# Performance work log

Hardware: AMD Instinct MI355X
Metric: run time of the kernel (lower is better)

## Reference

```python
import jax, jax.numpy as jnp
import numpy as np
import math

N = 8192
DIM = 256

def setup_inputs() -> dict:
    key = jax.random.key(0)
    k1, k2, k3 = jax.random.split(key, 3)
    h = jax.random.normal(k1, (N, DIM), dtype=jnp.float32)
    # xavier_uniform with gain=1.414 for square [dim, dim] matrices
    gain = 1.414
    bound = gain * math.sqrt(6.0 / (DIM + DIM))
    Wq = jax.random.uniform(k2, (DIM, DIM), dtype=jnp.float32, minval=-bound, maxval=bound)
    Wk = jax.random.uniform(k3, (DIM, DIM), dtype=jnp.float32, minval=-bound, maxval=bound)
    return {"h": h, "Wq": Wq, "Wk": Wk}

def reference(h, Wq, Wk):
    dim = h.shape[1]
    q = h @ Wq                                   # [N, dim]
    k = h @ Wk                                   # [N, dim]
    e = (q @ k.T) / jnp.sqrt(jnp.asarray(dim, h.dtype))  # [N, N]
    attention = jax.nn.softmax(e, axis=1)        # row-wise softmax
    attention = attention.mean(axis=0)           # [N], column-mean over rows
    x = attention @ h                            # [dim]
    return x
```

## Files before the change

### kernel.cpp

```cpp
#include <hip/hip_runtime.h>
#include <cstdint>
#include <cstddef>


#define N_ROWS 8192
#define DIM    256

typedef __bf16 bf16x8 __attribute__((ext_vector_type(8)));
typedef unsigned short u16x8 __attribute__((ext_vector_type(8)));
typedef float f32x16 __attribute__((ext_vector_type(16)));

__device__ __forceinline__ uint16_t f2bf(float f) {
    uint32_t u = __float_as_uint(f);
    uint32_t r = (u + 0x7fffu + ((u >> 16) & 1u)) >> 16;
    return (uint16_t)r;
}

__device__ __forceinline__ float fexp2(float x) {
#if __has_builtin(__builtin_amdgcn_exp2f)
    return __builtin_amdgcn_exp2f(x);
#else
    return __expf(x * 0.69314718056f);
#endif
}

__device__ __forceinline__ void gld16(const void* gsrc, void* ldst) {
    __builtin_amdgcn_global_load_lds(
        (const __attribute__((address_space(1))) unsigned int*)gsrc,
        (__attribute__((address_space(3))) unsigned int*)ldst, 16, 0, 0);
}

__global__ __launch_bounds__(256) void proj_kernel(
        const float* __restrict__ h, const float* __restrict__ Wq,
        const float* __restrict__ Wk, uint16_t* __restrict__ qf,
        uint16_t* __restrict__ kf, float* __restrict__ l_arr,
        float* __restrict__ c_arr, float* __restrict__ out) {
    __shared__ alignas(16) float hbf[32 * 260];
    __shared__ alignas(16) uint16_t rep[4][1024];
    const int tid = threadIdx.x, lane = tid & 63, wave = tid >> 6;
    const int bid = blockIdx.x;
    const int rt = bid >> 2, ph = bid & 3;
    const int which = ph >> 1, p = ph & 1;

    if (bid < 32)       l_arr[bid * 256 + tid] = 0.0f;
    else if (bid < 64)  c_arr[(bid - 32) * 256 + tid] = 0.0f;
    else if (bid == 64) out[tid] = 0.0f;

    const float* __restrict__ W = which ? Wk : Wq;
    uint16_t* __restrict__ dst = which ? kf : qf;
    const float scale = which ? 1.0f : (0.0625f * 1.44269504089f);

    for (int i = tid; i < 2048; i += 256) {
        int r = i >> 6, c = (i & 63) * 4;
        *(float4*)&hbf[r * 260 + c] = *(const float4*)&h[(size_t)(rt * 32 + r) * DIM + c];
    }
    __syncthreads();

    bf16x8 afrag[16];
    {
        const int r = lane & 31;
#pragma unroll
        for (int a0 = 0; a0 < 16; a0++) {
            const int c0 = a0 * 16 + (lane >> 5) * 8;
            float4 f0 = *(const float4*)&hbf[r * 260 + c0];
            float4 f1 = *(const float4*)&hbf[r * 260 + c0 + 4];
            u16x8 f;
            f[0] = f2bf(f0.x); f[1] = f2bf(f0.y); f[2] = f2bf(f0.z); f[3] = f2bf(f0.w);
            f[4] = f2bf(f1.x); f[5] = f2bf(f1.y); f[6] = f2bf(f1.z); f[7] = f2bf(f1.w);
            afrag[a0] = __builtin_bit_cast(bf16x8, f);
        }
    }

    const int ctl = wave;
    const int cl = ctl * 32 + (lane & 31);
    f32x16 acc;
#pragma unroll
    for (int i = 0; i < 16; i++) acc[i] = 0.0f;
#pragma unroll
    for (int a0 = 0; a0 < 16; a0++) {
        const int kb = a0 * 16 + (lane >> 5) * 8;
        u16x8 f;
#pragma unroll
        for (int j = 0; j < 8; j++)
            f[j] = f2bf(W[(size_t)(kb + j) * DIM + p * 128 + cl]);
        acc = __builtin_amdgcn_mfma_f32_32x32x16_bf16(
            afrag[a0], __builtin_bit_cast(bf16x8, f), acc, 0, 0, 0);
    }

    {
        const int dcl = lane & 31;
        const int a0o = dcl >> 4, hi = (dcl >> 3) & 1, jj = dcl & 7;
        const int ilb = 4 * (lane >> 5);
#pragma unroll
        for (int reg = 0; reg < 16; reg++) {
            int il = ilb + (reg & 3) + 8 * (reg >> 2);
            rep[wave][(size_t)((a0o * 64) + il + 32 * hi) * 8 + jj] =
                f2bf(acc[reg] * scale);
        }
        const uint4* rv = (const uint4*)&rep[wave][0];
        uint4* gp = (uint4*)(dst + (size_t)rt * 8192 +
                             (size_t)(p * 4 + ctl) * 1024);
        gp[lane * 2]     = rv[lane * 2];
        gp[lane * 2 + 1] = rv[lane * 2 + 1];
    }
}

template <int MODE>
__global__ __launch_bounds__(512, 2) void qk_pass(
        const uint16_t* __restrict__ qf, const uint16_t* __restrict__ kf,
        float* __restrict__ l_arr, float* __restrict__ c_arr) {
    __shared__ alignas(16) uint16_t ktile[2][16384];
    __shared__ float c_lds[512];
    const int tid = threadIdx.x, lane = tid & 63, wave = tid >> 6;
    const int bid = blockIdx.x;
    const int cc = bid & 15, rb = bid >> 4;
    const int t0 = rb * 16 + wave * 2;
    const int row0 = t0 * 32;

    const uint4* qp = (const uint4*)qf;
    bf16x8 q0[16], q1[16];
#pragma unroll
    for (int a0 = 0; a0 < 16; a0++) {
        q0[a0] = __builtin_bit_cast(bf16x8, qp[(size_t)t0 * 1024 + a0 * 64 + lane]);
        q1[a0] = __builtin_bit_cast(bf16x8, qp[(size_t)(t0 + 1) * 1024 + a0 * 64 + lane]);
    }

    float rs0[16], rs1[16];
    float rr0[16], rr1[16];
    if (MODE == 0) {
#pragma unroll
        for (int r = 0; r < 16; r++) { rs0[r] = 0.0f; rs1[r] = 0.0f; }
    } else {
#pragma unroll
        for (int r = 0; r < 16; r++) {
            int ro = (r & 3) + 8 * (r >> 2) + 4 * (lane >> 5);
            rr0[r] = 1.0f / (8192.0f * l_arr[row0 + ro]);
            rr1[r] = 1.0f / (8192.0f * l_arr[row0 + 32 + ro]);
        }
        if (tid < 512) c_lds[tid] = 0.0f;
    }

    const char* ksrc = (const char*)kf + (size_t)cc * 16 * 16384;

    {
        const char* s0 = ksrc + wave * 4096 + lane * 16;
        char* d0 = (char*)&ktile[0][0] + wave * 4096;
#pragma unroll
        for (int it = 0; it < 4; it++) gld16(s0 + it * 1024, d0 + it * 1024);
    }

    for (int g = 0; g < 8; g++) {
        __syncthreads();
        if (g < 7) {
            const char* sn = ksrc + (size_t)(2 * g + 2) * 16384 + wave * 4096 + lane * 16;
            char* dn = (char*)&ktile[(g + 1) & 1][0] + wave * 4096;
#pragma unroll
            for (int it = 0; it < 4; it++) gld16(sn + it * 1024, dn + it * 1024);
        }

#pragma unroll
        for (int sub = 0; sub < 2; sub++) {
            const int t = 2 * g + sub;
            const uint16_t* kt = &ktile[g & 1][sub * 8192];
            f32x16 acc0, acc1;
#pragma unroll
            for (int i = 0; i < 16; i++) { acc0[i] = 0.0f; acc1[i] = 0.0f; }
#pragma unroll
            for (int a0 = 0; a0 < 16; a0++) {
                bf16x8 b = __builtin_bit_cast(bf16x8,
                    *(const u16x8*)&kt[(size_t)(a0 * 64 + lane) * 8]);
                acc0 = __builtin_amdgcn_mfma_f32_32x32x16_bf16(q0[a0], b, acc0, 0, 0, 0);
                acc1 = __builtin_amdgcn_mfma_f32_32x32x16_bf16(q1[a0], b, acc1, 0, 0, 0);
            }

            if (MODE == 0) {
#pragma unroll
                for (int r = 0; r < 16; r++) {
                    rs0[r] += fexp2(acc0[r]);
                    rs1[r] += fexp2(acc1[r]);
                }
            } else {
                float sv = 0.0f;
#pragma unroll
                for (int r = 0; r < 16; r++) {
                    sv += fexp2(acc0[r]) * rr0[r];
                    sv += fexp2(acc1[r]) * rr1[r];
                }
                sv += __shfl_xor(sv, 32);
                if (lane < 32) atomicAdd(&c_lds[t * 32 + lane], sv);
            }
        }
    }

    if (MODE == 0) {
#pragma unroll
        for (int r = 0; r < 16; r++) {
            float v0 = rs0[r], v1 = rs1[r];
            v0 += __shfl_xor(v0, 1);  v0 += __shfl_xor(v0, 2);
            v0 += __shfl_xor(v0, 4);  v0 += __shfl_xor(v0, 8);
            v0 += __shfl_xor(v0, 16);
            v1 += __shfl_xor(v1, 1);  v1 += __shfl_xor(v1, 2);
            v1 += __shfl_xor(v1, 4);  v1 += __shfl_xor(v1, 8);
            v1 += __shfl_xor(v1, 16);
            if ((lane & 31) == 0) {
                int ro = (r & 3) + 8 * (r >> 2) + 4 * (lane >> 5);
                atomicAdd(&l_arr[row0 + ro], v0);
                atomicAdd(&l_arr[row0 + 32 + ro], v1);
            }
        }
    } else {
        __syncthreads();
        if (tid < 512) atomicAdd(&c_arr[cc * 512 + tid], c_lds[tid]);
    }
}

__global__ __launch_bounds__(256) void finish_kernel(
        const float* __restrict__ h, const float* __restrict__ c_arr,
        float* __restrict__ out) {
    const int d = threadIdx.x;
    const int j0 = blockIdx.x * 32;
    float acc = 0.0f;
#pragma unroll
    for (int jj = 0; jj < 32; jj++)
        acc += c_arr[j0 + jj] * h[(size_t)(j0 + jj) * DIM + d];
    atomicAdd(&out[d], acc);
}

extern "C" void kernel_launch(void* const* d_in, const int* in_sizes, int n_in,
                              void* d_out, int out_size, void* d_ws, size_t ws_size,
                              hipStream_t stream) {
    const float* h  = (const float*)d_in[0];
    const float* Wq = (const float*)d_in[1];
    const float* Wk = (const float*)d_in[2];

    uint16_t* qf = (uint16_t*)d_ws;
    uint16_t* kf = qf + (size_t)N_ROWS * DIM;
    float* l_arr = (float*)((char*)d_ws + (size_t)8 * 1024 * 1024);
    float* c_arr = l_arr + N_ROWS;
    float* out = (float*)d_out;

    proj_kernel<<<1024, 256, 0, stream>>>(h, Wq, Wk, qf, kf, l_arr, c_arr, out);
    qk_pass<0><<<256, 512, 0, stream>>>(qf, kf, l_arr, c_arr);
    qk_pass<1><<<256, 512, 0, stream>>>(qf, kf, l_arr, c_arr);
    finish_kernel<<<256, 256, 0, stream>>>(h, c_arr, out);
}
```

Measured before the change: 148.9 us.

## Store exp scores as fp16 matrix instead of recomputing QK^T in second pass

Replaces the two-pass scheme, which computed Q·K^T twice (once for row sums, once for the weighted column sums), with a single pass. That pass writes exp scores as an fp16 N×N matrix while it accumulates row sums. A new column-reduce kernel then reads the stored matrix, weights each entry by the inverse row sum, and accumulates column sums. This removes half of the MFMA work but adds a 128 MB write and read of the score matrix. The accumulators start at -9, a fixed exponent offset so values fit fp16, and values are clamped at 60000, which risks precision loss on large logits.

```diff
diff --git a/kernel.cpp b/kernel.cpp
--- a/kernel.cpp
+++ b/kernel.cpp
@@ -22,6 +22,13 @@
 #else
     return __expf(x * 0.69314718056f);
 #endif
+}
+
+__device__ __forceinline__ uint32_t pk_f16(float lo, float hi) {
+    union { _Float16 h[2]; uint32_t u; } v;
+    v.h[0] = (_Float16)lo;
+    v.h[1] = (_Float16)hi;
+    return v.u;
 }
 
 __device__ __forceinline__ void gld16(const void* gsrc, void* ldst) {
@@ -105,12 +112,10 @@
     }
 }
 
-template <int MODE>
-__global__ __launch_bounds__(512, 2) void qk_pass(
+__global__ __launch_bounds__(512, 2) void qk_store(
         const uint16_t* __restrict__ qf, const uint16_t* __restrict__ kf,
-        float* __restrict__ l_arr, float* __restrict__ c_arr) {
+        uint16_t* __restrict__ Pm, float* __restrict__ l_arr) {
     __shared__ alignas(16) uint16_t ktile[2][16384];
-    __shared__ float c_lds[512];
     const int tid = threadIdx.x, lane = tid & 63, wave = tid >> 6;
     const int bid = blockIdx.x;
     const int cc = bid & 15, rb = bid >> 4;
@@ -126,19 +131,11 @@
     }
 
     float rs0[16], rs1[16];
-    float rr0[16], rr1[16];
-    if (MODE == 0) {
-#pragma unroll
-        for (int r = 0; r < 16; r++) { rs0[r] = 0.0f; rs1[r] = 0.0f; }
-    } else {
-#pragma unroll
-        for (int r = 0; r < 16; r++) {
-            int ro = (r & 3) + 8 * (r >> 2) + 4 * (lane >> 5);
-            rr0[r] = 1.0f / (8192.0f * l_arr[row0 + ro]);
-            rr1[r] = 1.0f / (8192.0f * l_arr[row0 + 32 + ro]);
-        }
-        if (tid < 512) c_lds[tid] = 0.0f;
-    }
+#pragma unroll
+    for (int r = 0; r < 16; r++) { rs0[r] = 0.0f; rs1[r] = 0.0f; }
+
+    uint4* pst0 = (uint4*)(Pm + ((size_t)t0 * 256 + cc * 16) * 1024) + (size_t)lane * 2;
+    uint4* pst1 = pst0 + 256 * 128;
 
     const char* ksrc = (const char*)kf + (size_t)cc * 16 * 16384;
 
@@ -164,7 +161,7 @@
             const uint16_t* kt = &ktile[g & 1][sub * 8192];
             f32x16 acc0, acc1;
 #pragma unroll
-            for (int i = 0; i < 16; i++) { acc0[i] = 0.0f; acc1[i] = 0.0f; }
+            for (int i = 0; i < 16; i++) { acc0[i] = -9.0f; acc1[i] = -9.0f; }
 #pragma unroll
             for (int a0 = 0; a0 < 16; a0++) {
                 bf16x8 b = __builtin_bit_cast(bf16x8,
@@ -173,44 +170,96 @@
                 acc1 = __builtin_amdgcn_mfma_f32_32x32x16_bf16(q1[a0], b, acc1, 0, 0, 0);
             }
 
-            if (MODE == 0) {
-#pragma unroll
-                for (int r = 0; r < 16; r++) {
-                    rs0[r] += fexp2(acc0[r]);
-                    rs1[r] += fexp2(acc1[r]);
-                }
-            } else {
-                float sv = 0.0f;
-#pragma unroll
-                for (int r = 0; r < 16; r++) {
-                    sv += fexp2(acc0[r]) * rr0[r];
-                    sv += fexp2(acc1[r]) * rr1[r];
-                }
-                sv += __shfl_xor(sv, 32);
-                if (lane < 32) atomicAdd(&c_lds[t * 32 + lane], sv);
+            {
+                uint4 pw; float ea, eb;
+#define EPK(ACC, RS, J0, M)                                              \
+                ea = fminf(fexp2(ACC[J0]), 60000.0f);                    \
+                eb = fminf(fexp2(ACC[(J0) + 1]), 60000.0f);              \
+                RS[J0] += ea; RS[(J0) + 1] += eb;                        \
+                pw.M = pk_f16(ea, eb);
+                EPK(acc0, rs0, 0, x) EPK(acc0, rs0, 2, y)
+                EPK(acc0, rs0, 4, z) EPK(acc0, rs0, 6, w)
+                pst0[t * 128] = pw;
+                EPK(acc0, rs0, 8, x) EPK(acc0, rs0, 10, y)
+                EPK(acc0, rs0, 12, z) EPK(acc0, rs0, 14, w)
+                pst0[t * 128 + 1] = pw;
+                EPK(acc1, rs1, 0, x) EPK(acc1, rs1, 2, y)
+                EPK(acc1, rs1, 4, z) EPK(acc1, rs1, 6, w)
+                pst1[t * 128] = pw;
+                EPK(acc1, rs1, 8, x) EPK(acc1, rs1, 10, y)
+                EPK(acc1, rs1, 12, z) EPK(acc1, rs1, 14, w)
+                pst1[t * 128 + 1] = pw;
+#undef EPK
             }
         }
     }
 
-    if (MODE == 0) {
-#pragma unroll
-        for (int r = 0; r < 16; r++) {
-            float v0 = rs0[r], v1 = rs1[r];
-            v0 += __shfl_xor(v0, 1);  v0 += __shfl_xor(v0, 2);
-            v0 += __shfl_xor(v0, 4);  v0 += __shfl_xor(v0, 8);
-            v0 += __shfl_xor(v0, 16);
-            v1 += __shfl_xor(v1, 1);  v1 += __shfl_xor(v1, 2);
-            v1 += __shfl_xor(v1, 4);  v1 += __shfl_xor(v1, 8);
-            v1 += __shfl_xor(v1, 16);
-            if ((lane & 31) == 0) {
-                int ro = (r & 3) + 8 * (r >> 2) + 4 * (lane >> 5);
-                atomicAdd(&l_arr[row0 + ro], v0);
-                atomicAdd(&l_arr[row0 + 32 + ro], v1);
+#pragma unroll
+    for (int r = 0; r < 16; r++) {
+        float v0 = rs0[r], v1 = rs1[r];
+        v0 += __shfl_xor(v0, 1);  v0 += __shfl_xor(v0, 2);
+        v0 += __shfl_xor(v0, 4);  v0 += __shfl_xor(v0, 8);
+        v0 += __shfl_xor(v0, 16);
+        v1 += __shfl_xor(v1, 1);  v1 += __shfl_xor(v1, 2);
+        v1 += __shfl_xor(v1, 4);  v1 += __shfl_xor(v1, 8);
+        v1 += __shfl_xor(v1, 16);
+        if ((lane & 31) == 0) {
+            int ro = (r & 3) + 8 * (r >> 2) + 4 * (lane >> 5);
+            atomicAdd(&l_arr[row0 + ro], v0);
+            atomicAdd(&l_arr[row0 + 32 + ro], v1);
+        }
+    }
+}
+
+__global__ __launch_bounds__(512) void colreduce_kernel(
+        const uint16_t* __restrict__ Pm, const float* __restrict__ l_arr,
+        float* __restrict__ c_arr) {
+    __shared__ float wlds[128];
+    const int tid = threadIdx.x, lane = tid & 63, wave = tid >> 6;
+    const int bid = blockIdx.x;
+    const int cc = bid & 15, rg = bid >> 4;
+    if (tid < 128) wlds[tid] = 1.0f / (8192.0f * l_arr[rg * 128 + tid]);
+    __syncthreads();
+
+    const int rbase = 16 * (lane & 1);
+    float acc0 = 0.0f, acc1 = 0.0f;
+#pragma unroll
+    for (int t = 0; t < 4; t++) {
+        float wA[8], wB[8];
+#pragma unroll
+        for (int j = 0; j < 8; j++) {
+            const int r = (j & 3) + 8 * (j >> 2) + rbase;
+            wA[j] = wlds[t * 32 + r];
+            wB[j] = wlds[t * 32 + r + 4];
+        }
+        const size_t trow = (size_t)(rg * 4 + t) * 256;
+#pragma unroll
+        for (int c = 0; c < 2; c++) {
+            const uint4* up = (const uint4*)(Pm + (trow + cc * 16 + wave * 2 + c) * 1024);
+            uint4 v0 = up[lane];
+            uint4 v1 = up[lane + 64];
+            uint32_t a[4] = {v0.x, v0.y, v0.z, v0.w};
+            uint32_t b[4] = {v1.x, v1.y, v1.z, v1.w};
+            float s = 0.0f;
+#pragma unroll
+            for (int j = 0; j < 4; j++) {
+                union { uint32_t u; _Float16 h[2]; } ta, tb;
+                ta.u = a[j]; tb.u = b[j];
+                s += (float)ta.h[0] * wA[2 * j]
+                   + (float)ta.h[1] * wA[2 * j + 1]
+                   + (float)tb.h[0] * wB[2 * j]
+                   + (float)tb.h[1] * wB[2 * j + 1];
             }
-        }
-    } else {
-        __syncthreads();
-        if (tid < 512) atomicAdd(&c_arr[cc * 512 + tid], c_lds[tid]);
+            if (c == 0) acc0 += s; else acc1 += s;
+        }
+    }
+
+    acc0 += __shfl_xor(acc0, 1);
+    acc1 += __shfl_xor(acc1, 1);
+    if ((lane & 1) == 0) {
+        const int col = lane >> 1;
+        atomicAdd(&c_arr[cc * 512 + (wave * 2 + 0) * 32 + col], acc0);
+        atomicAdd(&c_arr[cc * 512 + (wave * 2 + 1) * 32 + col], acc1);
     }
 }
 
@@ -237,10 +286,11 @@
     uint16_t* kf = qf + (size_t)N_ROWS * DIM;
     float* l_arr = (float*)((char*)d_ws + (size_t)8 * 1024 * 1024);
     float* c_arr = l_arr + N_ROWS;
+    uint16_t* Pm = (uint16_t*)((char*)d_ws + (size_t)16 * 1024 * 1024);
     float* out = (float*)d_out;
 
     proj_kernel<<<1024, 256, 0, stream>>>(h, Wq, Wk, qf, kf, l_arr, c_arr, out);
-    qk_pass<0><<<256, 512, 0, stream>>>(qf, kf, l_arr, c_arr);
-    qk_pass<1><<<256, 512, 0, stream>>>(qf, kf, l_arr, c_arr);
+    qk_store<<<256, 512, 0, stream>>>(qf, kf, Pm, l_arr);
+    colreduce_kernel<<<1024, 512, 0, stream>>>(Pm, l_arr, c_arr);
     finish_kernel<<<256, 256, 0, stream>>>(h, c_arr, out);
 }
```

Result: slower. 185.3 us (+24.4%).

## Fuse two QK passes into one cooperative kernel with grid sync

Applied to the files above, without the earlier changes.

Merges the row-sum pass and the column-accumulation pass into a single cooperative kernel separated by a grid-wide barrier. Q fragments stay in registers across both phases, and the first K tile for the second pass is prefetched before the barrier. This removes one kernel launch and the reload of Q. In exchange it adds a grid sync and requires all 256 blocks to be co-resident.

```diff
diff --git a/kernel.cpp b/kernel.cpp
--- a/kernel.cpp
+++ b/kernel.cpp
@@ -1,6 +1,9 @@
 #include <hip/hip_runtime.h>
+#include <hip/hip_cooperative_groups.h>
 #include <cstdint>
 #include <cstddef>
+
+namespace cg = cooperative_groups;
 
 
 #define N_ROWS 8192
@@ -105,8 +108,7 @@
     }
 }
 
-template <int MODE>
-__global__ __launch_bounds__(512, 2) void qk_pass(
+__global__ __launch_bounds__(512, 2) void qk_fused(
         const uint16_t* __restrict__ qf, const uint16_t* __restrict__ kf,
         float* __restrict__ l_arr, float* __restrict__ c_arr) {
     __shared__ alignas(16) uint16_t ktile[2][16384];
@@ -125,42 +127,30 @@
         q1[a0] = __builtin_bit_cast(bf16x8, qp[(size_t)(t0 + 1) * 1024 + a0 * 64 + lane]);
     }
 
+    const char* ksrc = (const char*)kf + (size_t)cc * 16 * 16384;
+    const char* kwsrc = ksrc + wave * 4096 + lane * 16;
+    char* d0 = (char*)&ktile[0][0] + wave * 4096;
+    char* d1 = (char*)&ktile[1][0] + wave * 4096;
+
     float rs0[16], rs1[16];
-    float rr0[16], rr1[16];
-    if (MODE == 0) {
-#pragma unroll
-        for (int r = 0; r < 16; r++) { rs0[r] = 0.0f; rs1[r] = 0.0f; }
-    } else {
-#pragma unroll
-        for (int r = 0; r < 16; r++) {
-            int ro = (r & 3) + 8 * (r >> 2) + 4 * (lane >> 5);
-            rr0[r] = 1.0f / (8192.0f * l_arr[row0 + ro]);
-            rr1[r] = 1.0f / (8192.0f * l_arr[row0 + 32 + ro]);
-        }
-        if (tid < 512) c_lds[tid] = 0.0f;
-    }
-
-    const char* ksrc = (const char*)kf + (size_t)cc * 16 * 16384;
+#pragma unroll
+    for (int r = 0; r < 16; r++) { rs0[r] = 0.0f; rs1[r] = 0.0f; }
 
     {
-        const char* s0 = ksrc + wave * 4096 + lane * 16;
-        char* d0 = (char*)&ktile[0][0] + wave * 4096;
-#pragma unroll
-        for (int it = 0; it < 4; it++) gld16(s0 + it * 1024, d0 + it * 1024);
+#pragma unroll
+        for (int it = 0; it < 4; it++) gld16(kwsrc + it * 1024, d0 + it * 1024);
     }
 
     for (int g = 0; g < 8; g++) {
         __syncthreads();
         if (g < 7) {
-            const char* sn = ksrc + (size_t)(2 * g + 2) * 16384 + wave * 4096 + lane * 16;
-            char* dn = (char*)&ktile[(g + 1) & 1][0] + wave * 4096;
+            const char* sn = kwsrc + (size_t)(2 * g + 2) * 16384;
+            char* dn = (g & 1) ? d0 : d1;
 #pragma unroll
             for (int it = 0; it < 4; it++) gld16(sn + it * 1024, dn + it * 1024);
         }
-
 #pragma unroll
         for (int sub = 0; sub < 2; sub++) {
-            const int t = 2 * g + sub;
             const uint16_t* kt = &ktile[g & 1][sub * 8192];
             f32x16 acc0, acc1;
 #pragma unroll
@@ -172,46 +162,79 @@
                 acc0 = __builtin_amdgcn_mfma_f32_32x32x16_bf16(q0[a0], b, acc0, 0, 0, 0);
                 acc1 = __builtin_amdgcn_mfma_f32_32x32x16_bf16(q1[a0], b, acc1, 0, 0, 0);
             }
-
-            if (MODE == 0) {
-#pragma unroll
-                for (int r = 0; r < 16; r++) {
-                    rs0[r] += fexp2(acc0[r]);
-                    rs1[r] += fexp2(acc1[r]);
-                }
-            } else {
-                float sv = 0.0f;
-#pragma unroll
-                for (int r = 0; r < 16; r++) {
-                    sv += fexp2(acc0[r]) * rr0[r];
-                    sv += fexp2(acc1[r]) * rr1[r];
-                }
-                sv += __shfl_xor(sv, 32);
-                if (lane < 32) atomicAdd(&c_lds[t * 32 + lane], sv);
-            }
-        }
-    }
-
-    if (MODE == 0) {
-#pragma unroll
-        for (int r = 0; r < 16; r++) {
-            float v0 = rs0[r], v1 = rs1[r];
-            v0 += __shfl_xor(v0, 1);  v0 += __shfl_xor(v0, 2);
-            v0 += __shfl_xor(v0, 4);  v0 += __shfl_xor(v0, 8);
-            v0 += __shfl_xor(v0, 16);
-            v1 += __shfl_xor(v1, 1);  v1 += __shfl_xor(v1, 2);
-            v1 += __shfl_xor(v1, 4);  v1 += __shfl_xor(v1, 8);
-            v1 += __shfl_xor(v1, 16);
-            if ((lane & 31) == 0) {
-                int ro = (r & 3) + 8 * (r >> 2) + 4 * (lane >> 5);
-                atomicAdd(&l_arr[row0 + ro], v0);
-                atomicAdd(&l_arr[row0 + 32 + ro], v1);
-            }
-        }
-    } else {
+#pragma unroll
+            for (int r = 0; r < 16; r++) {
+                rs0[r] += fexp2(acc0[r]);
+                rs1[r] += fexp2(acc1[r]);
+            }
+        }
+    }
+
+#pragma unroll
+    for (int r = 0; r < 16; r++) {
+        float v0 = rs0[r], v1 = rs1[r];
+        v0 += __shfl_xor(v0, 1);  v0 += __shfl_xor(v0, 2);
+        v0 += __shfl_xor(v0, 4);  v0 += __shfl_xor(v0, 8);
+        v0 += __shfl_xor(v0, 16);
+        v1 += __shfl_xor(v1, 1);  v1 += __shfl_xor(v1, 2);
+        v1 += __shfl_xor(v1, 4);  v1 += __shfl_xor(v1, 8);
+        v1 += __shfl_xor(v1, 16);
+        if ((lane & 31) == 0) {
+            int ro = (r & 3) + 8 * (r >> 2) + 4 * (lane >> 5);
+            atomicAdd(&l_arr[row0 + ro], v0);
+            atomicAdd(&l_arr[row0 + 32 + ro], v1);
+        }
+    }
+
+#pragma unroll
+    for (int it = 0; it < 4; it++) gld16(kwsrc + it * 1024, d0 + it * 1024);
+
+    cg::this_grid().sync();
+
+    float rr0[16], rr1[16];
+#pragma unroll
+    for (int r = 0; r < 16; r++) {
+        int ro = (r & 3) + 8 * (r >> 2) + 4 * (lane >> 5);
+        rr0[r] = 1.0f / (8192.0f * l_arr[row0 + ro]);
+        rr1[r] = 1.0f / (8192.0f * l_arr[row0 + 32 + ro]);
+    }
+    c_lds[tid] = 0.0f;
+
+    for (int g = 0; g < 8; g++) {
         __syncthreads();
-        if (tid < 512) atomicAdd(&c_arr[cc * 512 + tid], c_lds[tid]);
-    }
+        if (g < 7) {
+            const char* sn = kwsrc + (size_t)(2 * g + 2) * 16384;
+            char* dn = (g & 1) ? d0 : d1;
+#pragma unroll
+            for (int it = 0; it < 4; it++) gld16(sn + it * 1024, dn + it * 1024);
+        }
+#pragma unroll
+        for (int sub = 0; sub < 2; sub++) {
+            const int t = 2 * g + sub;
+            const uint16_t* kt = &ktile[g & 1][sub * 8192];
+            f32x16 acc0, acc1;
+#pragma unroll
+            for (int i = 0; i < 16; i++) { acc0[i] = 0.0f; acc1[i] = 0.0f; }
+#pragma unroll
+            for (int a0 = 0; a0 < 16; a0++) {
+                bf16x8 b = __builtin_bit_cast(bf16x8,
+                    *(const u16x8*)&kt[(size_t)(a0 * 64 + lane) * 8]);
+                acc0 = __builtin_amdgcn_mfma_f32_32x32x16_bf16(q0[a0], b, acc0, 0, 0, 0);
+                acc1 = __builtin_amdgcn_mfma_f32_32x32x16_bf16(q1[a0], b, acc1, 0, 0, 0);
+            }
+            float sv = 0.0f;
+#pragma unroll
+            for (int r = 0; r < 16; r++) {
+                sv += fexp2(acc0[r]) * rr0[r];
+                sv += fexp2(acc1[r]) * rr1[r];
+            }
+            sv += __shfl_xor(sv, 32);
+            if (lane < 32) atomicAdd(&c_lds[t * 32 + lane], sv);
+        }
+    }
+
+    __syncthreads();
+    atomicAdd(&c_arr[cc * 512 + tid], c_lds[tid]);
 }
 
 __global__ __launch_bounds__(256) void finish_kernel(
@@ -240,7 +263,10 @@
     float* out = (float*)d_out;
 
     proj_kernel<<<1024, 256, 0, stream>>>(h, Wq, Wk, qf, kf, l_arr, c_arr, out);
-    qk_pass<0><<<256, 512, 0, stream>>>(qf, kf, l_arr, c_arr);
-    qk_pass<1><<<256, 512, 0, stream>>>(qf, kf, l_arr, c_arr);
+
+    void* args[] = {(void*)&qf, (void*)&kf, (void*)&l_arr, (void*)&c_arr};
+    hipLaunchCooperativeKernel((const void*)qk_fused, dim3(256), dim3(512),
+                               args, 0, stream);
+
     finish_kernel<<<256, 256, 0, stream>>>(h, c_arr, out);
 }
```

After: 193.2 us. +29.7%, slower.

## Deepen K-tile pipeline to 4 buffers and overlap softmax epilogue with MFMA

Applied to the files above, without the earlier changes.

Replaces the 2-stage, 2-tile-per-stage LDS double buffer in qk_pass with a 4-slot ring of single 32-column K tiles, prefetched two tiles ahead using explicit vmcnt waits and raw s_barrier. The exp/accumulate epilogue for the previous tile is deferred and interleaved with the current tile's LDS reads and MFMAs, and s_setprio raises wave priority around MFMA bursts. The launch-bounds minimum-blocks hint is dropped, which relaxes register pressure but may reduce occupancy. Correctness now relies on hand-counted vmcnt values and on a single barrier per tile guarding buffer reuse.

```diff
diff --git a/kernel.cpp b/kernel.cpp
--- a/kernel.cpp
+++ b/kernel.cpp
@@ -106,10 +106,10 @@
 }
 
 template <int MODE>
-__global__ __launch_bounds__(512, 2) void qk_pass(
+__global__ __launch_bounds__(512) void qk_pass(
         const uint16_t* __restrict__ qf, const uint16_t* __restrict__ kf,
         float* __restrict__ l_arr, float* __restrict__ c_arr) {
-    __shared__ alignas(16) uint16_t ktile[2][16384];
+    __shared__ alignas(16) uint16_t ktile[4][8192];
     __shared__ float c_lds[512];
     const int tid = threadIdx.x, lane = tid & 63, wave = tid >> 6;
     const int bid = blockIdx.x;
@@ -137,60 +137,85 @@
             rr0[r] = 1.0f / (8192.0f * l_arr[row0 + ro]);
             rr1[r] = 1.0f / (8192.0f * l_arr[row0 + 32 + ro]);
         }
-        if (tid < 512) c_lds[tid] = 0.0f;
+        c_lds[tid] = 0.0f;
     }
 
     const char* ksrc = (const char*)kf + (size_t)cc * 16 * 16384;
-
-    {
-        const char* s0 = ksrc + wave * 4096 + lane * 16;
-        char* d0 = (char*)&ktile[0][0] + wave * 4096;
-#pragma unroll
-        for (int it = 0; it < 4; it++) gld16(s0 + it * 1024, d0 + it * 1024);
-    }
-
-    for (int g = 0; g < 8; g++) {
-        __syncthreads();
-        if (g < 7) {
-            const char* sn = ksrc + (size_t)(2 * g + 2) * 16384 + wave * 4096 + lane * 16;
-            char* dn = (char*)&ktile[(g + 1) & 1][0] + wave * 4096;
-#pragma unroll
-            for (int it = 0; it < 4; it++) gld16(sn + it * 1024, dn + it * 1024);
-        }
-
-#pragma unroll
-        for (int sub = 0; sub < 2; sub++) {
-            const int t = 2 * g + sub;
-            const uint16_t* kt = &ktile[g & 1][sub * 8192];
-            f32x16 acc0, acc1;
-#pragma unroll
-            for (int i = 0; i < 16; i++) { acc0[i] = 0.0f; acc1[i] = 0.0f; }
-#pragma unroll
-            for (int a0 = 0; a0 < 16; a0++) {
-                bf16x8 b = __builtin_bit_cast(bf16x8,
-                    *(const u16x8*)&kt[(size_t)(a0 * 64 + lane) * 8]);
-                acc0 = __builtin_amdgcn_mfma_f32_32x32x16_bf16(q0[a0], b, acc0, 0, 0, 0);
-                acc1 = __builtin_amdgcn_mfma_f32_32x32x16_bf16(q1[a0], b, acc1, 0, 0, 0);
-            }
-
-            if (MODE == 0) {
-#pragma unroll
-                for (int r = 0; r < 16; r++) {
-                    rs0[r] += fexp2(acc0[r]);
-                    rs1[r] += fexp2(acc1[r]);
-                }
-            } else {
-                float sv = 0.0f;
-#pragma unroll
-                for (int r = 0; r < 16; r++) {
-                    sv += fexp2(acc0[r]) * rr0[r];
-                    sv += fexp2(acc1[r]) * rr1[r];
-                }
-                sv += __shfl_xor(sv, 32);
-                if (lane < 32) atomicAdd(&c_lds[t * 32 + lane], sv);
-            }
-        }
-    }
+    const char* kw = ksrc + wave * 2048 + lane * 16;
+
+#define STAGE(T) do {                                                        \
+        const char* _s = kw + (size_t)(T) * 16384;                           \
+        char* _d = (char*)&ktile[(T) & 3][0] + wave * 2048;                  \
+        gld16(_s, _d); gld16(_s + 1024, _d + 1024); } while (0)
+
+#define EPILOGUE(TPREV) do {                                                 \
+        if (MODE == 0) {                                                     \
+            _Pragma("unroll")                                                \
+            for (int r = 0; r < 16; r++) {                                   \
+                rs0[r] += fexp2(acc0[r]); rs1[r] += fexp2(acc1[r]);          \
+            }                                                                \
+        } else {                                                             \
+            float sv = 0.0f;                                                 \
+            _Pragma("unroll")                                                \
+            for (int r = 0; r < 16; r++) {                                   \
+                sv += fexp2(acc0[r]) * rr0[r];                               \
+                sv += fexp2(acc1[r]) * rr1[r];                               \
+            }                                                                \
+            sv += __shfl_xor(sv, 32);           \
+            if (lane < 32) atomicAdd(&c_lds[(TPREV) * 32 + lane], sv);       \
+        } } while (0)
+
+#define TILEBODY(T, DO_STAGE, DO_EPI, VM) do {                               \
+        asm volatile("s_waitcnt " VM ::: "memory");                          \
+        __builtin_amdgcn_s_barrier();                                        \
+        const uint16_t* kt = &ktile[(T) & 3][0];                             \
+        u16x8 b[8];                                                          \
+        _Pragma("unroll")                                                    \
+        for (int j = 0; j < 8; j++)                                          \
+            b[j] = *(const u16x8*)&kt[(size_t)(j * 64 + lane) * 8];          \
+        if (DO_STAGE) STAGE((T) + 2);                                        \
+        if (DO_EPI) EPILOGUE((T) - 1);                                       \
+        f32x16 na0, na1;                                                     \
+        _Pragma("unroll")                                                    \
+        for (int i = 0; i < 16; i++) { na0[i] = 0.0f; na1[i] = 0.0f; }       \
+        __builtin_amdgcn_s_setprio(1);                                       \
+        _Pragma("unroll")                                                    \
+        for (int j = 0; j < 8; j++) {                                        \
+            bf16x8 bb = __builtin_bit_cast(bf16x8, b[j]);                    \
+            na0 = __builtin_amdgcn_mfma_f32_32x32x16_bf16(q0[j], bb, na0, 0, 0, 0); \
+            na1 = __builtin_amdgcn_mfma_f32_32x32x16_bf16(q1[j], bb, na1, 0, 0, 0); \
+        }                                                                    \
+        __builtin_amdgcn_s_setprio(0);                                       \
+        _Pragma("unroll")                                                    \
+        for (int j = 0; j < 8; j++)                                          \
+            b[j] = *(const u16x8*)&kt[(size_t)((j + 8) * 64 + lane) * 8];    \
+        __builtin_amdgcn_s_setprio(1);                                       \
+        _Pragma("unroll")                                                    \
+        for (int j = 0; j < 8; j++) {                                        \
+            bf16x8 bb = __builtin_bit_cast(bf16x8, b[j]);                    \
+            na0 = __builtin_amdgcn_mfma_f32_32x32x16_bf16(q0[j + 8], bb, na0, 0, 0, 0); \
+            na1 = __builtin_amdgcn_mfma_f32_32x32x16_bf16(q1[j + 8], bb, na1, 0, 0, 0); \
+        }                                                                    \
+        __builtin_amdgcn_s_setprio(0);                                       \
+        acc0 = na0; acc1 = na1;                                              \
+    } while (0)
+
+    STAGE(0); STAGE(1);
+
+    f32x16 acc0, acc1;
+#pragma unroll
+    for (int i = 0; i < 16; i++) { acc0[i] = 0.0f; acc1[i] = 0.0f; }
+
+    TILEBODY(0, true, false, "vmcnt(2)");
+    for (int t = 1; t <= 13; t++)
+        TILEBODY(t, true, true, "vmcnt(2)");
+    TILEBODY(14, false, true, "vmcnt(2)");
+    TILEBODY(15, false, true, "vmcnt(0)");
+    EPILOGUE(15);
+
+#undef TILEBODY
+#undef EPILOGUE
+#undef STAGE
 
     if (MODE == 0) {
 #pragma unroll
@@ -210,7 +235,7 @@
         }
     } else {
         __syncthreads();
-        if (tid < 512) atomicAdd(&c_arr[cc * 512 + tid], c_lds[tid]);
+        atomicAdd(&c_arr[cc * 512 + tid], c_lds[tid]);
     }
 }
 
```

After: 159.6 us. 1.07x slower.
